# Optimization experiments

Measured on AMD Instinct MI355X. Metric: run time of the kernel, lower is better.

The kernel has to match this reference:

```python
import jax, jax.numpy as jnp
import numpy as np

B, T, C = 4, 2048, 1024
H, D = 16, 64          # n_head, head_size; H*D == C
FF = 4 * C             # compute_layer_scaling * n_embed
EPS = 1e-5


def layernorm(x, g, b):
    mu = jnp.mean(x, axis=-1, keepdims=True)
    var = jnp.var(x, axis=-1, keepdims=True)
    return (x - mu) * jax.lax.rsqrt(var + EPS) * g + b


def setup_inputs() -> dict:
    key = jax.random.key(0)
    ks = jax.random.split(key, 12)
    s_c = 1.0 / np.sqrt(C)
    s_ff = 1.0 / np.sqrt(FF)
    return {
        "x": jax.random.normal(ks[0], (B, T, C), dtype=jnp.float32),
        # per-head Q/K/V weights, stacked: [H, C, D] (Linear with bias=False)
        "Wq": jax.random.normal(ks[1], (H, C, D), dtype=jnp.float32) * s_c,
        "Wk": jax.random.normal(ks[2], (H, C, D), dtype=jnp.float32) * s_c,
        "Wv": jax.random.normal(ks[3], (H, C, D), dtype=jnp.float32) * s_c,
        "Wproj": jax.random.normal(ks[4], (C, C), dtype=jnp.float32) * s_c,
        "bproj": jnp.zeros((C,), dtype=jnp.float32),
        "W1": jax.random.normal(ks[5], (C, FF), dtype=jnp.float32) * s_c,
        "b1": jnp.zeros((FF,), dtype=jnp.float32),
        "W2": jax.random.normal(ks[6], (FF, FF), dtype=jnp.float32) * s_ff,
        "b2": jnp.zeros((FF,), dtype=jnp.float32),
        "W3": jax.random.normal(ks[7], (FF, C), dtype=jnp.float32) * s_ff,
        "b3": jnp.zeros((C,), dtype=jnp.float32),
        "ln1_g": jnp.ones((C,), dtype=jnp.float32),
        "ln1_b": jnp.zeros((C,), dtype=jnp.float32),
        "ln2_g": jnp.ones((C,), dtype=jnp.float32),
        "ln2_b": jnp.zeros((C,), dtype=jnp.float32),
    }


def reference(x, Wq, Wk, Wv, Wproj, bproj, W1, b1, W2, b2, W3, b3,
              ln1_g, ln1_b, ln2_g, ln2_b):
    # --- multi-head causal self-attention (pre-LN) ---
    h = layernorm(x, ln1_g, ln1_b)
    q = jnp.einsum("btc,hcd->bhtd", h, Wq)
    k = jnp.einsum("btc,hcd->bhtd", h, Wk)
    v = jnp.einsum("btc,hcd->bhtd", h, Wv)
    # NOTE: original scales by n_embed**-0.5 (C from x.shape), not head_size
    scores = jnp.einsum("bhtd,bhsd->bhts", q, k) * (C ** -0.5)
    causal = jnp.tril(jnp.ones((T, T), dtype=bool))
    scores = jnp.where(causal, scores, -jnp.inf)
    wei = jax.nn.softmax(scores, axis=-1)          # dropout p=0 -> identity
    attn = jnp.einsum("bhts,bhsd->bhtd", wei, v)
    attn = attn.transpose(0, 2, 1, 3).reshape(B, T, C)  # concat heads
    x = x + attn @ Wproj + bproj
    # --- feed-forward (pre-LN): C -> FF -> relu -> FF -> relu -> C ---
    h2 = layernorm(x, ln2_g, ln2_b)
    h2 = jax.nn.relu(h2 @ W1 + b1)
    h2 = jax.nn.relu(h2 @ W2 + b2)
    x = x + h2 @ W3 + b3
    return x
```

## Files before the change

kernel.cpp:

```cpp
#include <hip/hip_runtime.h>

typedef __bf16 bf16;
typedef bf16  bf16x8 __attribute__((ext_vector_type(8)));
typedef bf16  bf16x4 __attribute__((ext_vector_type(4)));
typedef float f32x4  __attribute__((ext_vector_type(4)));

#define T_SEQ 2048

__device__ __forceinline__ void gload_lds16(const bf16* g, bf16* l) {
    __builtin_amdgcn_global_load_lds(
        (const __attribute__((address_space(1))) unsigned int*)g,
        (__attribute__((address_space(3))) unsigned int*)l,
        16, 0, 0);
}

#define VMCNT(n) asm volatile("s_waitcnt vmcnt(" #n ")" ::: "memory")
#define BAR() do { asm volatile("" ::: "memory"); __builtin_amdgcn_s_barrier(); \
                   asm volatile("" ::: "memory"); } while (0)

__global__ __launch_bounds__(256) void transpose_f32_bf16(
    const float* __restrict__ in, bf16* __restrict__ out, int R, int Cc, int ldo)
{
    __shared__ float tile[32][33];
    const int bx = blockIdx.x * 32;
    const int by = blockIdx.y * 32;
    const long bi = (long)blockIdx.z * R * Cc;
    const long bo = (long)blockIdx.z * Cc * ldo;
    const int tx = threadIdx.x, ty = threadIdx.y;
#pragma unroll
    for (int i = 0; i < 4; ++i)
        tile[ty + i * 8][tx] = in[bi + (long)(by + ty + i * 8) * Cc + bx + tx];
    __syncthreads();
#pragma unroll
    for (int i = 0; i < 4; ++i)
        out[bo + (long)(bx + ty + i * 8) * ldo + by + tx] = (bf16)tile[tx][ty + i * 8];
}

__global__ __launch_bounds__(256) void transpose_bf16(
    const bf16* __restrict__ in, bf16* __restrict__ out, int ldi, int ldo)
{
    __shared__ bf16 tile[32][33];
    const int bx = blockIdx.x * 32;
    const int by = blockIdx.y * 32;
    const int tx = threadIdx.x, ty = threadIdx.y;
#pragma unroll
    for (int i = 0; i < 4; ++i)
        tile[ty + i * 8][tx] = in[(long)(by + ty + i * 8) * ldi + bx + tx];
    __syncthreads();
#pragma unroll
    for (int i = 0; i < 4; ++i)
        out[(long)(bx + ty + i * 8) * ldo + by + tx] = tile[tx][ty + i * 8];
}

__global__ __launch_bounds__(256) void ln_kernel(
    const float* __restrict__ x, const float* __restrict__ g,
    const float* __restrict__ bb, bf16* __restrict__ out)
{
    const long row = blockIdx.x;
    const int tid = threadIdx.x;
    const float4 v = ((const float4*)(x + row * 1024))[tid];
    float s  = v.x + v.y + v.z + v.w;
    float s2 = v.x * v.x + v.y * v.y + v.z * v.z + v.w * v.w;
#pragma unroll
    for (int off = 32; off >= 1; off >>= 1) {
        s  += __shfl_xor(s,  off, 64);
        s2 += __shfl_xor(s2, off, 64);
    }
    __shared__ float red[8];
    const int wid = tid >> 6;
    if ((tid & 63) == 0) { red[wid] = s; red[4 + wid] = s2; }
    __syncthreads();
    s  = red[0] + red[1] + red[2] + red[3];
    s2 = red[4] + red[5] + red[6] + red[7];
    const float mu   = s * (1.f / 1024.f);
    const float rstd = rsqrtf(s2 * (1.f / 1024.f) - mu * mu + 1e-5f);
    const float4 gv = ((const float4*)g)[tid];
    const float4 bv = ((const float4*)bb)[tid];
    bf16x4 ov;
    ov[0] = (bf16)((v.x - mu) * rstd * gv.x + bv.x);
    ov[1] = (bf16)((v.y - mu) * rstd * gv.y + bv.y);
    ov[2] = (bf16)((v.z - mu) * rstd * gv.z + bv.z);
    ov[3] = (bf16)((v.w - mu) * rstd * gv.w + bv.w);
    *(bf16x4*)(out + row * 1024 + tid * 4) = ov;
}

__global__ __launch_bounds__(256) void ln_kernel_b(
    const bf16* __restrict__ x, const float* __restrict__ g,
    const float* __restrict__ bb, bf16* __restrict__ out)
{
    const long row = blockIdx.x;
    const int tid = threadIdx.x;
    const bf16x4 vb = ((const bf16x4*)(x + row * 1024))[tid];
    const float v0 = (float)vb[0], v1 = (float)vb[1];
    const float v2 = (float)vb[2], v3 = (float)vb[3];
    float s  = v0 + v1 + v2 + v3;
    float s2 = v0 * v0 + v1 * v1 + v2 * v2 + v3 * v3;
#pragma unroll
    for (int off = 32; off >= 1; off >>= 1) {
        s  += __shfl_xor(s,  off, 64);
        s2 += __shfl_xor(s2, off, 64);
    }
    __shared__ float red[8];
    const int wid = tid >> 6;
    if ((tid & 63) == 0) { red[wid] = s; red[4 + wid] = s2; }
    __syncthreads();
    s  = red[0] + red[1] + red[2] + red[3];
    s2 = red[4] + red[5] + red[6] + red[7];
    const float mu   = s * (1.f / 1024.f);
    const float rstd = rsqrtf(s2 * (1.f / 1024.f) - mu * mu + 1e-5f);
    const float4 gv = ((const float4*)g)[tid];
    const float4 bv = ((const float4*)bb)[tid];
    bf16x4 ov;
    ov[0] = (bf16)((v0 - mu) * rstd * gv.x + bv.x);
    ov[1] = (bf16)((v1 - mu) * rstd * gv.y + bv.y);
    ov[2] = (bf16)((v2 - mu) * rstd * gv.z + bv.z);
    ov[3] = (bf16)((v3 - mu) * rstd * gv.w + bv.w);
    *(bf16x4*)(out + row * 1024 + tid * 4) = ov;
}

#define LOADA(BUFP, QM) do {                                                   \
    const char* ab_ = (BUFP) + (size_t)((wr * 64 + (QM) * 128 + fr) * 128);    \
    _Pragma("unroll") for (int m_ = 0; m_ < 4; ++m_) {                         \
        af[m_][0] = *(const bf16x8*)(ab_ + m_ * 2048 + so0);                   \
        af[m_][1] = *(const bf16x8*)(ab_ + m_ * 2048 + so1); } } while (0)

#define LOADB(BUFP, QN, DST) do {                                              \
    const char* bb_ = (BUFP) + (size_t)((wc * 32 + (QN) * 128 + fr) * 128);    \
    _Pragma("unroll") for (int n_ = 0; n_ < 2; ++n_) {                         \
        DST[n_][0] = *(const bf16x8*)(bb_ + n_ * 2048 + so0);                  \
        DST[n_][1] = *(const bf16x8*)(bb_ + n_ * 2048 + so1); } } while (0)

#define MMA(ACC, BSET) do { __builtin_amdgcn_s_setprio(1);                     \
    _Pragma("unroll") for (int m_ = 0; m_ < 4; ++m_)                           \
    _Pragma("unroll") for (int n_ = 0; n_ < 2; ++n_) {                         \
        ACC[m_][n_] = __builtin_amdgcn_mfma_f32_16x16x32_bf16(                 \
            af[m_][0], BSET[n_][0], ACC[m_][n_], 0, 0, 0);                     \
        ACC[m_][n_] = __builtin_amdgcn_mfma_f32_16x16x32_bf16(                 \
            af[m_][1], BSET[n_][1], ACC[m_][n_], 0, 0, 0); }                   \
    __builtin_amdgcn_s_setprio(0); } while (0)

#define TB_DEEP(W1N, W3N, ISSN, ISSC) do {                                     \
    const char* abuf = cAs + ((size_t)cur << 15);                              \
    const char* bbuf = cBs + ((size_t)cur << 15);                              \
    const long kb  = (long)(k + 1) * 64;                                       \
    const long kb2 = (long)(k + 2) * 64;                                       \
    LOADA(abuf, 0);                                                            \
    LOADB(bbuf, 0, bfv0);                                                      \
    if (ISSN) stageB(nxt, 0, kb);                                 \
    BAR(); MMA(a00, bfv0); BAR();                                              \
    LOADB(bbuf, 1, bfv1);                                                      \
    if (ISSN) stageA(nxt, 1, kb);                                 \
    VMCNT(W1N);                                                                \
    BAR(); MMA(a01, bfv1); BAR();                                              \
    LOADA(abuf, 1);                                                            \
    if (ISSC) stageA(cur, 0, kb2);                                \
    BAR(); MMA(a11, bfv1); BAR();                                              \
    if (ISSC) stageB(cur, 1, kb2);                                \
    VMCNT(W3N);                                                                \
    BAR(); MMA(a10, bfv0); BAR(); } while (0)

template <int MODE>
__global__ __launch_bounds__(512, 1) void gemm256(
    const bf16* __restrict__ A, const bf16* __restrict__ Bt,
    const float* __restrict__ bias, const float* __restrict__ resid,
    void* __restrict__ outp, int M, int N, int K, int nbn)
{
    extern __shared__ __align__(16) char smem[];
    char* cAs = smem;
    char* cBs = smem + 65536;

    const int tid = threadIdx.x;
    const int wid = tid >> 6, lane = tid & 63;
    const int wr = wid >> 2, wc = wid & 3;
    const int fr = lane & 15, fq = lane >> 4;

    const int nwg = gridDim.x;
    const int cpx = nwg >> 3;
    const int b0  = blockIdx.x;
    const int bid = (b0 & 7) * cpx + (b0 >> 3);
    const long bm = bid / nbn, bn = bid % nbn;
    const long bmrow = bm * 256, bnrow = bn * 256;

    const int srow0 = wid * 8 + (lane >> 3);
    const int sslot = (lane & 7) ^ (lane >> 3);
    auto stageA = [&](int buf, int h, long kt) {
        const bf16* g = A + (size_t)(bmrow + h * 128 + srow0) * K + kt + sslot * 8;
        char* l = cAs + ((size_t)buf << 15) + h * 16384 + (size_t)wid * 1024;
        gload_lds16(g, (bf16*)l);
        gload_lds16(g + (size_t)64 * K, (bf16*)(l + 8192));
    };
    auto stageB = [&](int buf, int h, long kt) {
        const bf16* g = Bt + (size_t)(bnrow + h * 128 + srow0) * K + kt + sslot * 8;
        char* l = cBs + ((size_t)buf << 15) + h * 16384 + (size_t)wid * 1024;
        gload_lds16(g, (bf16*)l);
        gload_lds16(g + (size_t)64 * K, (bf16*)(l + 8192));
    };

    const int sx  = fr & 7;
    const int so0 = ((fq) ^ sx) * 16;
    const int so1 = ((4 + fq) ^ sx) * 16;

    bf16x8 af[4][2], bfv0[2][2], bfv1[2][2];
    f32x4 a00[4][2], a01[4][2], a11[4][2], a10[4][2];
#pragma unroll
    for (int m = 0; m < 4; ++m)
#pragma unroll
        for (int n = 0; n < 2; ++n) {
            a00[m][n] = {0.f, 0.f, 0.f, 0.f}; a01[m][n] = {0.f, 0.f, 0.f, 0.f};
            a11[m][n] = {0.f, 0.f, 0.f, 0.f}; a10[m][n] = {0.f, 0.f, 0.f, 0.f};
        }

    stageA(0, 0, 0);
    stageB(0, 1, 0);
    stageB(0, 0, 0);
    stageA(0, 1, 0);
    stageA(1, 0, 64);
    stageB(1, 1, 64);
    VMCNT(6);
    BAR();

    const int NT = K >> 6;
    int cur, nxt;
    int k = 0;
    for (; k < NT - 2; ++k) {
        cur = k & 1; nxt = cur ^ 1;
        TB_DEEP(8, 6, true, true);
    }
    cur = k & 1; nxt = cur ^ 1;
    TB_DEEP(8, 2, true, false);
    ++k;
    cur = k & 1; nxt = cur ^ 1;
    TB_DEEP(0, 0, false, false);

    auto writeQ = [&](f32x4 (&acc)[4][2], int QM, int QN) {
#pragma unroll
        for (int m = 0; m < 4; ++m) {
            const long row0 = bmrow + wr * 64 + QM * 128 + m * 16 + fq * 4;
#pragma unroll
            for (int n = 0; n < 2; ++n) {
                const long col = bnrow + wc * 32 + QN * 128 + n * 16 + fr;
                const float bv = (MODE == 0) ? 0.f : bias[col];
#pragma unroll
                for (int j = 0; j < 4; ++j) {
                    const long row = row0 + j;
                    float v = acc[m][n][j] + bv;
                    if (MODE == 1) v = fmaxf(v, 0.f);
                    if (MODE == 2) {
                        v += resid[row * N + col];
                        ((float*)outp)[row * N + col] = v;
                    } else {
                        ((bf16*)outp)[row * N + col] = (bf16)v;
                    }
                }
            }
        }
    };
    writeQ(a00, 0, 0); writeQ(a01, 0, 1); writeQ(a11, 1, 1); writeQ(a10, 1, 0);
}

#define TILE_BODY_N(PRE, LAST) do {                                            \
    const char* abuf = cAs + ((size_t)cur << 15);                              \
    const char* bbuf = cBs + ((size_t)cur << 14);                              \
    const long kn = (long)(k + 1) * 64;                                        \
    LOADA(abuf, 0);                                                            \
    LOADB(bbuf, 0, bfv);                                                       \
    if (PRE) { stageA(nxt, 0, kn); stageB(nxt, kn); stageA(nxt, 1, kn);        \
               VMCNT(6); }                                                     \
    else     { VMCNT(0); }                                                     \
    BAR(); MMA(aq0, bfv); BAR();                                               \
    LOADA(abuf, 1);                                                            \
    if (PRE) { VMCNT(2); }                                                     \
    if (!LAST) { BAR(); }                                                      \
    MMA(aq1, bfv);                                                             \
    if (!LAST) { BAR(); } } while (0)

template <int MODE>
__global__ __launch_bounds__(512, 2) void gemm256n(
    const bf16* __restrict__ A, const bf16* __restrict__ Bt,
    const float* __restrict__ bias, const void* __restrict__ resid,
    void* __restrict__ outp, int M, int N, int K, int nbn)
{
    extern __shared__ __align__(16) char smem[];
    char* cAs = smem;
    char* cBs = smem + 65536;

    const int tid = threadIdx.x;
    const int wid = tid >> 6, lane = tid & 63;
    const int wr = wid >> 2, wc = wid & 3;
    const int fr = lane & 15, fq = lane >> 4;

    const int nwg = gridDim.x;
    const int cpx = nwg >> 3;
    const int b0  = blockIdx.x;
    const int bid = (b0 & 7) * cpx + (b0 >> 3);
    const long bm = bid / nbn, bn = bid % nbn;
    const long bmrow = bm * 256, bnrow = bn * 128;

    const int srow0 = wid * 8 + (lane >> 3);
    const int sslot = (lane & 7) ^ (lane >> 3);
    auto stageA = [&](int buf, int h, long kt) {
        const bf16* g = A + (size_t)(bmrow + h * 128 + srow0) * K + kt + sslot * 8;
        char* l = cAs + ((size_t)buf << 15) + h * 16384 + (size_t)wid * 1024;
        gload_lds16(g, (bf16*)l);
        gload_lds16(g + (size_t)64 * K, (bf16*)(l + 8192));
    };
    auto stageB = [&](int buf, long kt) {
        const bf16* g = Bt + (size_t)(bnrow + srow0) * K + kt + sslot * 8;
        char* l = cBs + ((size_t)buf << 14) + (size_t)wid * 1024;
        gload_lds16(g, (bf16*)l);
        gload_lds16(g + (size_t)64 * K, (bf16*)(l + 8192));
    };

    const int sx  = fr & 7;
    const int so0 = ((fq) ^ sx) * 16;
    const int so1 = ((4 + fq) ^ sx) * 16;

    bf16x8 af[4][2], bfv[2][2];
    f32x4 aq0[4][2], aq1[4][2];
#pragma unroll
    for (int m = 0; m < 4; ++m)
#pragma unroll
        for (int n = 0; n < 2; ++n) {
            aq0[m][n] = {0.f, 0.f, 0.f, 0.f};
            aq1[m][n] = {0.f, 0.f, 0.f, 0.f};
        }

    stageA(0, 0, 0); stageB(0, 0); stageA(0, 1, 0);
    VMCNT(2);
    BAR();

    const int NT = K >> 6;
    int cur = 0, nxt = 1;
    int k = 0;
    for (; k < NT - 1; ++k) {
        cur = k & 1; nxt = cur ^ 1;
        TILE_BODY_N(true, false);
    }
    cur = k & 1; nxt = cur ^ 1;
    TILE_BODY_N(false, true);

    auto writeQ = [&](f32x4 (&acc)[4][2], int QM) {
#pragma unroll
        for (int m = 0; m < 4; ++m) {
            const long row0 = bmrow + wr * 64 + QM * 128 + m * 16 + fq * 4;
#pragma unroll
            for (int n = 0; n < 2; ++n) {
                const long col = bnrow + wc * 32 + n * 16 + fr;
                const float bv = (MODE == 0) ? 0.f : bias[col];
#pragma unroll
                for (int j = 0; j < 4; ++j) {
                    const long row = row0 + j;
                    float v = acc[m][n][j] + bv;
                    if (MODE == 3) {
                        v += ((const float*)resid)[row * N + col];
                        ((bf16*)outp)[row * N + col] = (bf16)v;
                    } else if (MODE == 4) {
                        v += (float)((const bf16*)resid)[row * N + col];
                        ((float*)outp)[row * N + col] = v;
                    } else {
                        ((bf16*)outp)[row * N + col] = (bf16)v;
                    }
                }
            }
        }
    };
    writeQ(aq0, 0); writeQ(aq1, 1);
}

__device__ __forceinline__ void sm_part(
    f32x4* s, float* mj, f32x4* o, f32x4& o_l, bf16* Pp,
    int fr, int fq, int qloc, bool diag)
{
    float v[4][4], mxj[4];
#pragma unroll
    for (int j = 0; j < 4; ++j) {
        const int qg = qloc + fq * 4 + j;
        v[0][j] = s[0][j] * 0.03125f;
        v[1][j] = s[1][j] * 0.03125f;
        v[2][j] = s[2][j] * 0.03125f;
        v[3][j] = s[3][j] * 0.03125f;
        if (diag) {
            if (fr      > qg) v[0][j] = -1e30f;
            if (16 + fr > qg) v[1][j] = -1e30f;
            if (32 + fr > qg) v[2][j] = -1e30f;
            if (48 + fr > qg) v[3][j] = -1e30f;
        }
        float mx = fmaxf(fmaxf(v[0][j], v[1][j]), fmaxf(v[2][j], v[3][j]));
#pragma unroll
        for (int off = 1; off <= 8; off <<= 1) mx = fmaxf(mx, __shfl_xor(mx, off, 16));
        mxj[j] = mx;
    }
    float need = fmaxf(fmaxf(mxj[0] - mj[0], mxj[1] - mj[1]),
                       fmaxf(mxj[2] - mj[2], mxj[3] - mj[3]));
    if (__any(need > 8.f)) {
#pragma unroll
        for (int j = 0; j < 4; ++j) {
            const float mn   = fmaxf(mj[j], mxj[j]);
            const float corr = __expf(mj[j] - mn);
            mj[j] = mn;
#pragma unroll
            for (int nd = 0; nd < 4; ++nd) o[nd][j] *= corr;
            o_l[j] *= corr;
        }
    }
#pragma unroll
    for (int j = 0; j < 4; ++j) {
        bf16* prow = Pp + (fq * 4 + j) * 72;
        prow[fr]      = (bf16)__expf(v[0][j] - mj[j]);
        prow[16 + fr] = (bf16)__expf(v[1][j] - mj[j]);
        prow[32 + fr] = (bf16)__expf(v[2][j] - mj[j]);
        prow[48 + fr] = (bf16)__expf(v[3][j] - mj[j]);
    }
}

__device__ __forceinline__ void attn_step(
    const bf16* __restrict__ Ks, const bf16* __restrict__ Vt,
    bf16* __restrict__ Pp, const bf16x8* qf,
    f32x4* o, f32x4& o_l, float* mj, const bf16x8 onesf,
    int fr, int fq, int qloc, bool diag)
{
    f32x4 s[4];
#pragma unroll
    for (int n = 0; n < 4; ++n) s[n] = {0.f, 0.f, 0.f, 0.f};
    __builtin_amdgcn_s_setprio(1);
#pragma unroll
    for (int n = 0; n < 4; ++n) {
        const int t  = n * 16 + fr;
        const int sw = ((t ^ (t >> 3)) & 7) << 4;
        const bf16x8 kf0 = *(const bf16x8*)((const char*)Ks + t * 128 + ((fq * 16) ^ sw));
        const bf16x8 kf1 = *(const bf16x8*)((const char*)Ks + t * 128 + ((64 + fq * 16) ^ sw));
        s[n] = __builtin_amdgcn_mfma_f32_16x16x32_bf16(qf[0], kf0, s[n], 0, 0, 0);
        s[n] = __builtin_amdgcn_mfma_f32_16x16x32_bf16(qf[1], kf1, s[n], 0, 0, 0);
    }
    __builtin_amdgcn_s_setprio(0);
    sm_part(s, mj, o, o_l, Pp, fr, fq, qloc, diag);
    asm volatile("s_waitcnt lgkmcnt(0)" ::: "memory");
    __builtin_amdgcn_sched_barrier(0);
    const bf16x8 pf0 = *(const bf16x8*)(Pp + fr * 72 + fq * 8);
    const bf16x8 pf1 = *(const bf16x8*)(Pp + fr * 72 + 32 + fq * 8);
    __builtin_amdgcn_s_setprio(1);
#pragma unroll
    for (int nd = 0; nd < 4; ++nd) {
        const int dd = nd * 16 + fr;
        const int sw = ((dd ^ (dd >> 3)) & 7) << 4;
        const bf16x8 vf0 = *(const bf16x8*)((const char*)Vt + dd * 128 + ((fq * 16) ^ sw));
        const bf16x8 vf1 = *(const bf16x8*)((const char*)Vt + dd * 128 + ((64 + fq * 16) ^ sw));
        o[nd] = __builtin_amdgcn_mfma_f32_16x16x32_bf16(pf0, vf0, o[nd], 0, 0, 0);
        o[nd] = __builtin_amdgcn_mfma_f32_16x16x32_bf16(pf1, vf1, o[nd], 0, 0, 0);
    }
    o_l = __builtin_amdgcn_mfma_f32_16x16x32_bf16(pf0, onesf, o_l, 0, 0, 0);
    o_l = __builtin_amdgcn_mfma_f32_16x16x32_bf16(pf1, onesf, o_l, 0, 0, 0);
    __builtin_amdgcn_s_setprio(0);
}

__device__ __forceinline__ void attn_step2(
    const bf16* __restrict__ Ks, const bf16* __restrict__ Vt,
    bf16* __restrict__ PpA, bf16* __restrict__ PpB,
    const bf16x8* qfA, const bf16x8* qfB,
    f32x4* oA, f32x4& olA, float* mA,
    f32x4* oB, f32x4& olB, float* mB,
    const bf16x8 onesf, int fr, int fq, int qloc, bool diagA)
{
    f32x4 sA[4], sB[4];
#pragma unroll
    for (int n = 0; n < 4; ++n) { sA[n] = {0.f, 0.f, 0.f, 0.f}; sB[n] = {0.f, 0.f, 0.f, 0.f}; }
    __builtin_amdgcn_s_setprio(1);
#pragma unroll
    for (int n = 0; n < 4; ++n) {
        const int t  = n * 16 + fr;
        const int sw = ((t ^ (t >> 3)) & 7) << 4;
        const bf16x8 kf0 = *(const bf16x8*)((const char*)Ks + t * 128 + ((fq * 16) ^ sw));
        const bf16x8 kf1 = *(const bf16x8*)((const char*)Ks + t * 128 + ((64 + fq * 16) ^ sw));
        sA[n] = __builtin_amdgcn_mfma_f32_16x16x32_bf16(qfA[0], kf0, sA[n], 0, 0, 0);
        sA[n] = __builtin_amdgcn_mfma_f32_16x16x32_bf16(qfA[1], kf1, sA[n], 0, 0, 0);
        sB[n] = __builtin_amdgcn_mfma_f32_16x16x32_bf16(qfB[0], kf0, sB[n], 0, 0, 0);
        sB[n] = __builtin_amdgcn_mfma_f32_16x16x32_bf16(qfB[1], kf1, sB[n], 0, 0, 0);
    }
    __builtin_amdgcn_s_setprio(0);
    sm_part(sA, mA, oA, olA, PpA, fr, fq, qloc, diagA);
    sm_part(sB, mB, oB, olB, PpB, fr, fq, qloc, false);
    asm volatile("s_waitcnt lgkmcnt(0)" ::: "memory");
    __builtin_amdgcn_sched_barrier(0);
    const bf16x8 pfA0 = *(const bf16x8*)(PpA + fr * 72 + fq * 8);
    const bf16x8 pfA1 = *(const bf16x8*)(PpA + fr * 72 + 32 + fq * 8);
    const bf16x8 pfB0 = *(const bf16x8*)(PpB + fr * 72 + fq * 8);
    const bf16x8 pfB1 = *(const bf16x8*)(PpB + fr * 72 + 32 + fq * 8);
    __builtin_amdgcn_s_setprio(1);
#pragma unroll
    for (int nd = 0; nd < 4; ++nd) {
        const int dd = nd * 16 + fr;
        const int sw = ((dd ^ (dd >> 3)) & 7) << 4;
        const bf16x8 vf0 = *(const bf16x8*)((const char*)Vt + dd * 128 + ((fq * 16) ^ sw));
        const bf16x8 vf1 = *(const bf16x8*)((const char*)Vt + dd * 128 + ((64 + fq * 16) ^ sw));
        oA[nd] = __builtin_amdgcn_mfma_f32_16x16x32_bf16(pfA0, vf0, oA[nd], 0, 0, 0);
        oA[nd] = __builtin_amdgcn_mfma_f32_16x16x32_bf16(pfA1, vf1, oA[nd], 0, 0, 0);
        oB[nd] = __builtin_amdgcn_mfma_f32_16x16x32_bf16(pfB0, vf0, oB[nd], 0, 0, 0);
        oB[nd] = __builtin_amdgcn_mfma_f32_16x16x32_bf16(pfB1, vf1, oB[nd], 0, 0, 0);
    }
    olA = __builtin_amdgcn_mfma_f32_16x16x32_bf16(pfA0, onesf, olA, 0, 0, 0);
    olA = __builtin_amdgcn_mfma_f32_16x16x32_bf16(pfA1, onesf, olA, 0, 0, 0);
    olB = __builtin_amdgcn_mfma_f32_16x16x32_bf16(pfB0, onesf, olB, 0, 0, 0);
    olB = __builtin_amdgcn_mfma_f32_16x16x32_bf16(pfB1, onesf, olB, 0, 0, 0);
    __builtin_amdgcn_s_setprio(0);
}

__global__ __launch_bounds__(256) void attn_kernel(
    const bf16* __restrict__ qkv, const bf16* __restrict__ vt,
    bf16* __restrict__ out)
{
    const int pair = blockIdx.x;
    const int h = blockIdx.y, b = blockIdx.z;
    const int tid = threadIdx.x, wid = tid >> 6, lane = tid & 63;
    const int fr = lane & 15, fq = lane >> 4;
    const int jA = pair, jB = 31 - pair;
    const bf16* baseQ = qkv + ((long)b * T_SEQ) * 3072 + h * 64;
    const bf16* baseK = baseQ + 1024;
    const bf16* baseV = vt + (long)(h * 64) * 8192 + (long)b * T_SEQ;

    __shared__ __align__(16) bf16 Ks[2][64 * 64];
    __shared__ __align__(16) bf16 Vs[2][64 * 64];
    __shared__ __align__(16) bf16 Plds[2][4][16 * 72];

    const int qrA = jA * 64 + wid * 16 + fr;
    const int qrB = jB * 64 + wid * 16 + fr;
    bf16x8 qfA[2], qfB[2];
#pragma unroll
    for (int kk = 0; kk < 2; ++kk) {
        qfA[kk] = *(const bf16x8*)(baseQ + (long)qrA * 3072 + kk * 32 + fq * 8);
        qfB[kk] = *(const bf16x8*)(baseQ + (long)qrB * 3072 + kk * 32 + fq * 8);
    }

    bf16x8 onesf;
    {
        const bf16 ov = (fr == 0) ? (bf16)1.f : (bf16)0.f;
#pragma unroll
        for (int e = 0; e < 8; ++e) onesf[e] = ov;
    }

    f32x4 oA[4], oB[4], olA, olB;
    float mA[4], mB[4];
#pragma unroll
    for (int nd = 0; nd < 4; ++nd) { oA[nd] = {0.f, 0.f, 0.f, 0.f}; oB[nd] = {0.f, 0.f, 0.f, 0.f}; }
    olA = {0.f, 0.f, 0.f, 0.f}; olB = {0.f, 0.f, 0.f, 0.f};
#pragma unroll
    for (int j = 0; j < 4; ++j) { mA[j] = -1e30f; mB[j] = -1e30f; }

    const int t_p0 = wid * 16 + (lane >> 3);
    const int t_p1 = t_p0 + 8;
    const int kcb0 = ((lane & 7) * 16) ^ (((t_p0 ^ (t_p0 >> 3)) & 7) << 4);
    const int kcb1 = ((lane & 7) * 16) ^ (((t_p1 ^ (t_p1 >> 3)) & 7) << 4);

    bf16* PA = &Plds[0][wid][0];
    bf16* PB = &Plds[1][wid][0];

    auto stage = [&](int buf, int c) {
        const long s0 = (long)c * 64;
        gload_lds16(baseK + (s0 + t_p0) * 3072 + (kcb0 >> 1), &Ks[buf][(wid * 2) * 512]);
        gload_lds16(baseK + (s0 + t_p1) * 3072 + (kcb1 >> 1), &Ks[buf][(wid * 2 + 1) * 512]);
        gload_lds16(baseV + (long)t_p0 * 8192 + s0 + (kcb0 >> 1), &Vs[buf][(wid * 2) * 512]);
        gload_lds16(baseV + (long)t_p1 * 8192 + s0 + (kcb1 >> 1), &Vs[buf][(wid * 2 + 1) * 512]);
    };

    const int nch = jB + 1;
    stage(0, 0);
    for (int c = 0; c < nch; ++c) {
        const int cur = c & 1;
        if (c + 1 < nch) { stage(cur ^ 1, c + 1); VMCNT(4); }
        else             { VMCNT(0); }
        BAR();
        if (c <= jA)
            attn_step2(Ks[cur], Vs[cur], PA, PB, qfA, qfB,
                       oA, olA, mA, oB, olB, mB, onesf, fr, fq, wid * 16, c == jA);
        else
            attn_step(Ks[cur], Vs[cur], PB, qfB, oB, olB, mB, onesf,
                      fr, fq, wid * 16, c == jB);
        BAR();
    }

#pragma unroll
    for (int j = 0; j < 4; ++j) {
        const float lA = __shfl(olA[j], lane & 48, 64);
        const float lB = __shfl(olB[j], lane & 48, 64);
        const float rA = 1.f / lA, rB = 1.f / lB;
        const long rowA = (long)b * T_SEQ + jA * 64 + wid * 16 + fq * 4 + j;
        const long rowB = (long)b * T_SEQ + jB * 64 + wid * 16 + fq * 4 + j;
#pragma unroll
        for (int nd = 0; nd < 4; ++nd) {
            out[rowA * 1024 + h * 64 + nd * 16 + fr] = (bf16)(oA[nd][j] * rA);
            out[rowB * 1024 + h * 64 + nd * 16 + fr] = (bf16)(oB[nd][j] * rB);
        }
    }
}

extern "C" void kernel_launch(void* const* d_in, const int* in_sizes, int n_in,
                              void* d_out, int out_size, void* d_ws, size_t ws_size,
                              hipStream_t stream)
{
    const float* x     = (const float*)d_in[0];
    const float* Wq    = (const float*)d_in[1];
    const float* Wk    = (const float*)d_in[2];
    const float* Wv    = (const float*)d_in[3];
    const float* Wproj = (const float*)d_in[4];
    const float* bproj = (const float*)d_in[5];
    const float* W1    = (const float*)d_in[6];
    const float* b1    = (const float*)d_in[7];
    const float* W2    = (const float*)d_in[8];
    const float* b2    = (const float*)d_in[9];
    const float* W3    = (const float*)d_in[10];
    const float* b3    = (const float*)d_in[11];
    const float* ln1g  = (const float*)d_in[12];
    const float* ln1b  = (const float*)d_in[13];
    const float* ln2g  = (const float*)d_in[14];
    const float* ln2b  = (const float*)d_in[15];

    char* ws = (char*)d_ws;
    size_t off = 0;
    auto alloc = [&](size_t bytes) {
        void* p = ws + off;
        off += (bytes + 255) & ~(size_t)255;
        return p;
    };
    bf16* Wqkv_t  = (bf16*)alloc(3072ul * 1024 * 2);
    bf16* Wproj_t = (bf16*)alloc(1024ul * 1024 * 2);
    bf16* W1_t    = (bf16*)alloc(4096ul * 1024 * 2);
    bf16* W2_t    = (bf16*)alloc(4096ul * 4096 * 2);
    bf16* W3_t    = (bf16*)alloc(1024ul * 4096 * 2);
    bf16* hbuf    = (bf16*)alloc(8192ul * 1024 * 2);
    bf16* x1b     = (bf16*)alloc(8192ul * 1024 * 2);
    bf16* a1      = (bf16*)alloc(8192ul * 4096 * 2);
    char* R1      = (char*)alloc(8192ul * 4096 * 2);
    bf16* qkvb    = (bf16*)R1;
    bf16* attnb   = (bf16*)(R1 + 8192ul * 3072 * 2);
    bf16* a2      = (bf16*)R1;
    bf16* vt      = a1;

    hipFuncSetAttribute(reinterpret_cast<const void*>(&gemm256<1>),
                        hipFuncAttributeMaxDynamicSharedMemorySize, 131072);
    hipFuncSetAttribute(reinterpret_cast<const void*>(&gemm256n<0>),
                        hipFuncAttributeMaxDynamicSharedMemorySize, 98304);
    hipFuncSetAttribute(reinterpret_cast<const void*>(&gemm256n<3>),
                        hipFuncAttributeMaxDynamicSharedMemorySize, 98304);
    hipFuncSetAttribute(reinterpret_cast<const void*>(&gemm256n<4>),
                        hipFuncAttributeMaxDynamicSharedMemorySize, 98304);

    const dim3 tb(32, 8);
    transpose_f32_bf16<<<dim3(2, 32, 16), tb, 0, stream>>>(Wq, Wqkv_t,                1024, 64, 1024);
    transpose_f32_bf16<<<dim3(2, 32, 16), tb, 0, stream>>>(Wk, Wqkv_t + 1024l * 1024, 1024, 64, 1024);
    transpose_f32_bf16<<<dim3(2, 32, 16), tb, 0, stream>>>(Wv, Wqkv_t + 2048l * 1024, 1024, 64, 1024);
    transpose_f32_bf16<<<dim3(32, 32, 1),   tb, 0, stream>>>(Wproj, Wproj_t, 1024, 1024, 1024);
    transpose_f32_bf16<<<dim3(128, 32, 1),  tb, 0, stream>>>(W1, W1_t, 1024, 4096, 1024);
    transpose_f32_bf16<<<dim3(128, 128, 1), tb, 0, stream>>>(W2, W2_t, 4096, 4096, 4096);
    transpose_f32_bf16<<<dim3(32, 128, 1),  tb, 0, stream>>>(W3, W3_t, 4096, 1024, 4096);

    ln_kernel<<<8192, 256, 0, stream>>>(x, ln1g, ln1b, hbuf);
    gemm256n<0><<<768, 512, 98304, stream>>>(hbuf, Wqkv_t, nullptr, nullptr, qkvb,
                                             8192, 3072, 1024, 24);
    transpose_bf16<<<dim3(32, 256), tb, 0, stream>>>(qkvb + 2048, vt, 3072, 8192);
    attn_kernel<<<dim3(16, 16, 4), 256, 0, stream>>>(qkvb, vt, attnb);
    gemm256n<3><<<256, 512, 98304, stream>>>(attnb, Wproj_t, bproj, x, x1b,
                                             8192, 1024, 1024, 8);
    ln_kernel_b<<<8192, 256, 0, stream>>>(x1b, ln2g, ln2b, hbuf);
    gemm256<1><<<512, 512, 131072, stream>>>(hbuf, W1_t, b1, nullptr, a1,
                                             8192, 4096, 1024, 16);
    gemm256<1><<<512, 512, 131072, stream>>>(a1, W2_t, b2, nullptr, a2,
                                             8192, 4096, 4096, 16);
    gemm256n<4><<<256, 512, 98304, stream>>>(a2, W3_t, b3, x1b, (float*)d_out,
                                             8192, 1024, 4096, 8);
}
```

Baseline: 665.5 us.

## Process two causal query-tile pairs per attention block to reuse K/V tiles

Each attention block now handles four query tiles (two balanced causal pairs) sharing the same staged K/V chunks, halving the grid and the K/V load traffic. P scratch moves to dynamic shared memory sized for four tiles. This raises register and LDS use per block, which may reduce occupancy and parallelism with only 512 blocks.

Result: slower. 730.2 us (+9.7%).

```diff
diff --git a/kernel.cpp b/kernel.cpp
--- a/kernel.cpp
+++ b/kernel.cpp
@@ -508,26 +508,28 @@
     const bf16* __restrict__ qkv, const bf16* __restrict__ vt,
     bf16* __restrict__ out)
 {
-    const int pair = blockIdx.x;
+    const int p = blockIdx.x;
     const int h = blockIdx.y, b = blockIdx.z;
     const int tid = threadIdx.x, wid = tid >> 6, lane = tid & 63;
     const int fr = lane & 15, fq = lane >> 4;
-    const int jA = pair, jB = 31 - pair;
+    const int jA1 = p, jB1 = 31 - p;
+    const int jA2 = p + 8, jB2 = 23 - p;
     const bf16* baseQ = qkv + ((long)b * T_SEQ) * 3072 + h * 64;
     const bf16* baseK = baseQ + 1024;
     const bf16* baseV = vt + (long)(h * 64) * 8192 + (long)b * T_SEQ;
 
-    __shared__ __align__(16) bf16 Ks[2][64 * 64];
-    __shared__ __align__(16) bf16 Vs[2][64 * 64];
-    __shared__ __align__(16) bf16 Plds[2][4][16 * 72];
-
-    const int qrA = jA * 64 + wid * 16 + fr;
-    const int qrB = jB * 64 + wid * 16 + fr;
-    bf16x8 qfA[2], qfB[2];
+    extern __shared__ __align__(16) char asmem[];
+    bf16* Ks = (bf16*)asmem;
+    bf16* Vs = (bf16*)(asmem + 16384);
+    bf16* Pl = (bf16*)(asmem + 32768);
+
+    bf16x8 qfA1[2], qfB1[2], qfA2[2], qfB2[2];
 #pragma unroll
     for (int kk = 0; kk < 2; ++kk) {
-        qfA[kk] = *(const bf16x8*)(baseQ + (long)qrA * 3072 + kk * 32 + fq * 8);
-        qfB[kk] = *(const bf16x8*)(baseQ + (long)qrB * 3072 + kk * 32 + fq * 8);
+        qfA1[kk] = *(const bf16x8*)(baseQ + (long)(jA1 * 64 + wid * 16 + fr) * 3072 + kk * 32 + fq * 8);
+        qfB1[kk] = *(const bf16x8*)(baseQ + (long)(jB1 * 64 + wid * 16 + fr) * 3072 + kk * 32 + fq * 8);
+        qfA2[kk] = *(const bf16x8*)(baseQ + (long)(jA2 * 64 + wid * 16 + fr) * 3072 + kk * 32 + fq * 8);
+        qfB2[kk] = *(const bf16x8*)(baseQ + (long)(jB2 * 64 + wid * 16 + fr) * 3072 + kk * 32 + fq * 8);
     }
 
     bf16x8 onesf;
@@ -537,59 +539,74 @@
         for (int e = 0; e < 8; ++e) onesf[e] = ov;
     }
 
-    f32x4 oA[4], oB[4], olA, olB;
-    float mA[4], mB[4];
-#pragma unroll
-    for (int nd = 0; nd < 4; ++nd) { oA[nd] = {0.f, 0.f, 0.f, 0.f}; oB[nd] = {0.f, 0.f, 0.f, 0.f}; }
-    olA = {0.f, 0.f, 0.f, 0.f}; olB = {0.f, 0.f, 0.f, 0.f};
-#pragma unroll
-    for (int j = 0; j < 4; ++j) { mA[j] = -1e30f; mB[j] = -1e30f; }
+    f32x4 oA1[4], oB1[4], oA2[4], oB2[4], olA1, olB1, olA2, olB2;
+    float mA1[4], mB1[4], mA2[4], mB2[4];
+#pragma unroll
+    for (int nd = 0; nd < 4; ++nd) {
+        oA1[nd] = {0.f, 0.f, 0.f, 0.f}; oB1[nd] = {0.f, 0.f, 0.f, 0.f};
+        oA2[nd] = {0.f, 0.f, 0.f, 0.f}; oB2[nd] = {0.f, 0.f, 0.f, 0.f};
+    }
+    olA1 = {0.f, 0.f, 0.f, 0.f}; olB1 = {0.f, 0.f, 0.f, 0.f};
+    olA2 = {0.f, 0.f, 0.f, 0.f}; olB2 = {0.f, 0.f, 0.f, 0.f};
+#pragma unroll
+    for (int j = 0; j < 4; ++j) { mA1[j] = -1e30f; mB1[j] = -1e30f;
+                                  mA2[j] = -1e30f; mB2[j] = -1e30f; }
 
     const int t_p0 = wid * 16 + (lane >> 3);
     const int t_p1 = t_p0 + 8;
     const int kcb0 = ((lane & 7) * 16) ^ (((t_p0 ^ (t_p0 >> 3)) & 7) << 4);
     const int kcb1 = ((lane & 7) * 16) ^ (((t_p1 ^ (t_p1 >> 3)) & 7) << 4);
 
-    bf16* PA = &Plds[0][wid][0];
-    bf16* PB = &Plds[1][wid][0];
+    bf16* PA1 = Pl + (0 * 4 + wid) * 1152;
+    bf16* PB1 = Pl + (1 * 4 + wid) * 1152;
+    bf16* PA2 = Pl + (2 * 4 + wid) * 1152;
+    bf16* PB2 = Pl + (3 * 4 + wid) * 1152;
 
     auto stage = [&](int buf, int c) {
         const long s0 = (long)c * 64;
-        gload_lds16(baseK + (s0 + t_p0) * 3072 + (kcb0 >> 1), &Ks[buf][(wid * 2) * 512]);
-        gload_lds16(baseK + (s0 + t_p1) * 3072 + (kcb1 >> 1), &Ks[buf][(wid * 2 + 1) * 512]);
-        gload_lds16(baseV + (long)t_p0 * 8192 + s0 + (kcb0 >> 1), &Vs[buf][(wid * 2) * 512]);
-        gload_lds16(baseV + (long)t_p1 * 8192 + s0 + (kcb1 >> 1), &Vs[buf][(wid * 2 + 1) * 512]);
-    };
-
-    const int nch = jB + 1;
+        gload_lds16(baseK + (s0 + t_p0) * 3072 + (kcb0 >> 1), Ks + buf * 4096 + (wid * 2) * 512);
+        gload_lds16(baseK + (s0 + t_p1) * 3072 + (kcb1 >> 1), Ks + buf * 4096 + (wid * 2 + 1) * 512);
+        gload_lds16(baseV + (long)t_p0 * 8192 + s0 + (kcb0 >> 1), Vs + buf * 4096 + (wid * 2) * 512);
+        gload_lds16(baseV + (long)t_p1 * 8192 + s0 + (kcb1 >> 1), Vs + buf * 4096 + (wid * 2 + 1) * 512);
+    };
+
+    const int nch = jB1 + 1;
     stage(0, 0);
     for (int c = 0; c < nch; ++c) {
         const int cur = c & 1;
         if (c + 1 < nch) { stage(cur ^ 1, c + 1); VMCNT(4); }
         else             { VMCNT(0); }
         BAR();
-        if (c <= jA)
-            attn_step2(Ks[cur], Vs[cur], PA, PB, qfA, qfB,
-                       oA, olA, mA, oB, olB, mB, onesf, fr, fq, wid * 16, c == jA);
+        const bf16* Kc = Ks + cur * 4096;
+        const bf16* Vc = Vs + cur * 4096;
+        if (c <= jA1)
+            attn_step2(Kc, Vc, PA1, PB1, qfA1, qfB1,
+                       oA1, olA1, mA1, oB1, olB1, mB1, onesf, fr, fq, wid * 16, c == jA1);
         else
-            attn_step(Ks[cur], Vs[cur], PB, qfB, oB, olB, mB, onesf,
-                      fr, fq, wid * 16, c == jB);
+            attn_step(Kc, Vc, PB1, qfB1, oB1, olB1, mB1, onesf,
+                      fr, fq, wid * 16, c == jB1);
+        if (c <= jA2)
+            attn_step2(Kc, Vc, PA2, PB2, qfA2, qfB2,
+                       oA2, olA2, mA2, oB2, olB2, mB2, onesf, fr, fq, wid * 16, c == jA2);
+        else if (c <= jB2)
+            attn_step(Kc, Vc, PB2, qfB2, oB2, olB2, mB2, onesf,
+                      fr, fq, wid * 16, c == jB2);
         BAR();
     }
 
-#pragma unroll
-    for (int j = 0; j < 4; ++j) {
-        const float lA = __shfl(olA[j], lane & 48, 64);
-        const float lB = __shfl(olB[j], lane & 48, 64);
-        const float rA = 1.f / lA, rB = 1.f / lB;
-        const long rowA = (long)b * T_SEQ + jA * 64 + wid * 16 + fq * 4 + j;
-        const long rowB = (long)b * T_SEQ + jB * 64 + wid * 16 + fq * 4 + j;
-#pragma unroll
-        for (int nd = 0; nd < 4; ++nd) {
-            out[rowA * 1024 + h * 64 + nd * 16 + fr] = (bf16)(oA[nd][j] * rA);
-            out[rowB * 1024 + h * 64 + nd * 16 + fr] = (bf16)(oB[nd][j] * rB);
+    auto writeO = [&](f32x4* o, f32x4& ol, int jq) {
+#pragma unroll
+        for (int j = 0; j < 4; ++j) {
+            const float l = __shfl(ol[j], lane & 48, 64);
+            const float r = 1.f / l;
+            const long row = (long)b * T_SEQ + jq * 64 + wid * 16 + fq * 4 + j;
+#pragma unroll
+            for (int nd = 0; nd < 4; ++nd)
+                out[row * 1024 + h * 64 + nd * 16 + fr] = (bf16)(o[nd][j] * r);
         }
-    }
+    };
+    writeO(oA1, olA1, jA1); writeO(oB1, olB1, jB1);
+    writeO(oA2, olA2, jA2); writeO(oB2, olB2, jB2);
 }
 
 extern "C" void kernel_launch(void* const* d_in, const int* in_sizes, int n_in,
@@ -642,6 +659,8 @@
                         hipFuncAttributeMaxDynamicSharedMemorySize, 98304);
     hipFuncSetAttribute(reinterpret_cast<const void*>(&gemm256n<4>),
                         hipFuncAttributeMaxDynamicSharedMemorySize, 98304);
+    hipFuncSetAttribute(reinterpret_cast<const void*>(&attn_kernel),
+                        hipFuncAttributeMaxDynamicSharedMemorySize, 69632);
 
     const dim3 tb(32, 8);
     transpose_f32_bf16<<<dim3(2, 32, 16), tb, 0, stream>>>(Wq, Wqkv_t,                1024, 64, 1024);
@@ -656,7 +675,7 @@
     gemm256n<0><<<768, 512, 98304, stream>>>(hbuf, Wqkv_t, nullptr, nullptr, qkvb,
                                              8192, 3072, 1024, 24);
     transpose_bf16<<<dim3(32, 256), tb, 0, stream>>>(qkvb + 2048, vt, 3072, 8192);
-    attn_kernel<<<dim3(16, 16, 4), 256, 0, stream>>>(qkvb, vt, attnb);
+    attn_kernel<<<dim3(8, 16, 4), 256, 69632, stream>>>(qkvb, vt, attnb);
     gemm256n<3><<<256, 512, 98304, stream>>>(attnb, Wproj_t, bproj, x, x1b,
                                              8192, 1024, 1024, 8);
     ln_kernel_b<<<8192, 256, 0, stream>>>(x1b, ln2g, ln2b, hbuf);
```

## Fuse V transpose into QKV GEMM epilogue and shrink attention P buffer

Applied to the files above, without the earlier changes.

The QKV GEMM gains a new epilogue mode that writes the V columns directly in transposed layout, which removes the separate bf16 transpose kernel and its extra memory round trip. In attention, the per-wave P scratch is halved to a single buffer that the A and B query halves reuse one after the other, and it now uses an XOR-swizzled 128-byte row layout instead of padded rows. Launch bounds request 4 blocks per CU, aiming for higher occupancy. The transposed V stores from the GEMM are strided, so they are uncoalesced, and reusing one P buffer serialises the two softmax passes.

Result: slower. 893.6 us (+34.3%).

```diff
diff --git a/kernel.cpp b/kernel.cpp
--- a/kernel.cpp
+++ b/kernel.cpp
@@ -34,22 +34,6 @@
 #pragma unroll
     for (int i = 0; i < 4; ++i)
         out[bo + (long)(bx + ty + i * 8) * ldo + by + tx] = (bf16)tile[tx][ty + i * 8];
-}
-
-__global__ __launch_bounds__(256) void transpose_bf16(
-    const bf16* __restrict__ in, bf16* __restrict__ out, int ldi, int ldo)
-{
-    __shared__ bf16 tile[32][33];
-    const int bx = blockIdx.x * 32;
-    const int by = blockIdx.y * 32;
-    const int tx = threadIdx.x, ty = threadIdx.y;
-#pragma unroll
-    for (int i = 0; i < 4; ++i)
-        tile[ty + i * 8][tx] = in[(long)(by + ty + i * 8) * ldi + bx + tx];
-    __syncthreads();
-#pragma unroll
-    for (int i = 0; i < 4; ++i)
-        out[(long)(bx + ty + i * 8) * ldo + by + tx] = tile[tx][ty + i * 8];
 }
 
 __global__ __launch_bounds__(256) void ln_kernel(
@@ -346,7 +330,7 @@
 #pragma unroll
             for (int n = 0; n < 2; ++n) {
                 const long col = bnrow + wc * 32 + n * 16 + fr;
-                const float bv = (MODE == 0) ? 0.f : bias[col];
+                const float bv = (MODE == 0 || MODE == 5) ? 0.f : bias[col];
 #pragma unroll
                 for (int j = 0; j < 4; ++j) {
                     const long row = row0 + j;
@@ -357,6 +341,11 @@
                     } else if (MODE == 4) {
                         v += (float)((const bf16*)resid)[row * N + col];
                         ((float*)outp)[row * N + col] = v;
+                    } else if (MODE == 5) {
+                        if (col < 2048)
+                            ((bf16*)outp)[row * N + col] = (bf16)v;
+                        else
+                            ((bf16*)resid)[(col - 2048) * 8192 + row] = (bf16)v;
                     } else {
                         ((bf16*)outp)[row * N + col] = (bf16)v;
                     }
@@ -405,13 +394,20 @@
     }
 #pragma unroll
     for (int j = 0; j < 4; ++j) {
-        bf16* prow = Pp + (fq * 4 + j) * 72;
-        prow[fr]      = (bf16)__expf(v[0][j] - mj[j]);
-        prow[16 + fr] = (bf16)__expf(v[1][j] - mj[j]);
-        prow[32 + fr] = (bf16)__expf(v[2][j] - mj[j]);
-        prow[48 + fr] = (bf16)__expf(v[3][j] - mj[j]);
-    }
-}
+        const int r = fq * 4 + j;
+        char* prow = (char*)Pp + r * 128;
+        const int sw = (r & 7) << 4;
+        *(bf16*)(prow + ((fr * 2) ^ sw))      = (bf16)__expf(v[0][j] - mj[j]);
+        *(bf16*)(prow + ((32 + fr * 2) ^ sw)) = (bf16)__expf(v[1][j] - mj[j]);
+        *(bf16*)(prow + ((64 + fr * 2) ^ sw)) = (bf16)__expf(v[2][j] - mj[j]);
+        *(bf16*)(prow + ((96 + fr * 2) ^ sw)) = (bf16)__expf(v[3][j] - mj[j]);
+    }
+}
+
+#define PLOAD(P0, P1, PP) do {                                                 \
+    const int swr_ = (fr & 7) << 4;                                            \
+    P0 = *(const bf16x8*)((const char*)(PP) + fr * 128 + ((fq * 16) ^ swr_));  \
+    P1 = *(const bf16x8*)((const char*)(PP) + fr * 128 + ((64 + fq * 16) ^ swr_)); } while (0)
 
 __device__ __forceinline__ void attn_step(
     const bf16* __restrict__ Ks, const bf16* __restrict__ Vt,
@@ -436,8 +432,8 @@
     sm_part(s, mj, o, o_l, Pp, fr, fq, qloc, diag);
     asm volatile("s_waitcnt lgkmcnt(0)" ::: "memory");
     __builtin_amdgcn_sched_barrier(0);
-    const bf16x8 pf0 = *(const bf16x8*)(Pp + fr * 72 + fq * 8);
-    const bf16x8 pf1 = *(const bf16x8*)(Pp + fr * 72 + 32 + fq * 8);
+    bf16x8 pf0, pf1;
+    PLOAD(pf0, pf1, Pp);
     __builtin_amdgcn_s_setprio(1);
 #pragma unroll
     for (int nd = 0; nd < 4; ++nd) {
@@ -455,7 +451,7 @@
 
 __device__ __forceinline__ void attn_step2(
     const bf16* __restrict__ Ks, const bf16* __restrict__ Vt,
-    bf16* __restrict__ PpA, bf16* __restrict__ PpB,
+    bf16* __restrict__ Pp,
     const bf16x8* qfA, const bf16x8* qfB,
     f32x4* oA, f32x4& olA, float* mA,
     f32x4* oB, f32x4& olB, float* mB,
@@ -477,14 +473,16 @@
         sB[n] = __builtin_amdgcn_mfma_f32_16x16x32_bf16(qfB[1], kf1, sB[n], 0, 0, 0);
     }
     __builtin_amdgcn_s_setprio(0);
-    sm_part(sA, mA, oA, olA, PpA, fr, fq, qloc, diagA);
-    sm_part(sB, mB, oB, olB, PpB, fr, fq, qloc, false);
+    sm_part(sA, mA, oA, olA, Pp, fr, fq, qloc, diagA);
     asm volatile("s_waitcnt lgkmcnt(0)" ::: "memory");
     __builtin_amdgcn_sched_barrier(0);
-    const bf16x8 pfA0 = *(const bf16x8*)(PpA + fr * 72 + fq * 8);
-    const bf16x8 pfA1 = *(const bf16x8*)(PpA + fr * 72 + 32 + fq * 8);
-    const bf16x8 pfB0 = *(const bf16x8*)(PpB + fr * 72 + fq * 8);
-    const bf16x8 pfB1 = *(const bf16x8*)(PpB + fr * 72 + 32 + fq * 8);
+    bf16x8 pfA0, pfA1;
+    PLOAD(pfA0, pfA1, Pp);
+    sm_part(sB, mB, oB, olB, Pp, fr, fq, qloc, false);
+    asm volatile("s_waitcnt lgkmcnt(0)" ::: "memory");
+    __builtin_amdgcn_sched_barrier(0);
+    bf16x8 pfB0, pfB1;
+    PLOAD(pfB0, pfB1, Pp);
     __builtin_amdgcn_s_setprio(1);
 #pragma unroll
     for (int nd = 0; nd < 4; ++nd) {
@@ -504,7 +502,7 @@
     __builtin_amdgcn_s_setprio(0);
 }
 
-__global__ __launch_bounds__(256) void attn_kernel(
+__global__ __launch_bounds__(256, 4) void attn_kernel(
     const bf16* __restrict__ qkv, const bf16* __restrict__ vt,
     bf16* __restrict__ out)
 {
@@ -519,7 +517,7 @@
 
     __shared__ __align__(16) bf16 Ks[2][64 * 64];
     __shared__ __align__(16) bf16 Vs[2][64 * 64];
-    __shared__ __align__(16) bf16 Plds[2][4][16 * 72];
+    __shared__ __align__(16) bf16 Pl[4][1024];
 
     const int qrA = jA * 64 + wid * 16 + fr;
     const int qrB = jB * 64 + wid * 16 + fr;
@@ -550,8 +548,7 @@
     const int kcb0 = ((lane & 7) * 16) ^ (((t_p0 ^ (t_p0 >> 3)) & 7) << 4);
     const int kcb1 = ((lane & 7) * 16) ^ (((t_p1 ^ (t_p1 >> 3)) & 7) << 4);
 
-    bf16* PA = &Plds[0][wid][0];
-    bf16* PB = &Plds[1][wid][0];
+    bf16* P = &Pl[wid][0];
 
     auto stage = [&](int buf, int c) {
         const long s0 = (long)c * 64;
@@ -569,10 +566,10 @@
         else             { VMCNT(0); }
         BAR();
         if (c <= jA)
-            attn_step2(Ks[cur], Vs[cur], PA, PB, qfA, qfB,
+            attn_step2(Ks[cur], Vs[cur], P, qfA, qfB,
                        oA, olA, mA, oB, olB, mB, onesf, fr, fq, wid * 16, c == jA);
         else
-            attn_step(Ks[cur], Vs[cur], PB, qfB, oB, olB, mB, onesf,
+            attn_step(Ks[cur], Vs[cur], P, qfB, oB, olB, mB, onesf,
                       fr, fq, wid * 16, c == jB);
         BAR();
     }
@@ -636,7 +633,7 @@
 
     hipFuncSetAttribute(reinterpret_cast<const void*>(&gemm256<1>),
                         hipFuncAttributeMaxDynamicSharedMemorySize, 131072);
-    hipFuncSetAttribute(reinterpret_cast<const void*>(&gemm256n<0>),
+    hipFuncSetAttribute(reinterpret_cast<const void*>(&gemm256n<5>),
                         hipFuncAttributeMaxDynamicSharedMemorySize, 98304);
     hipFuncSetAttribute(reinterpret_cast<const void*>(&gemm256n<3>),
                         hipFuncAttributeMaxDynamicSharedMemorySize, 98304);
@@ -653,9 +650,8 @@
     transpose_f32_bf16<<<dim3(32, 128, 1),  tb, 0, stream>>>(W3, W3_t, 4096, 1024, 4096);
 
     ln_kernel<<<8192, 256, 0, stream>>>(x, ln1g, ln1b, hbuf);
-    gemm256n<0><<<768, 512, 98304, stream>>>(hbuf, Wqkv_t, nullptr, nullptr, qkvb,
+    gemm256n<5><<<768, 512, 98304, stream>>>(hbuf, Wqkv_t, nullptr, vt, qkvb,
                                              8192, 3072, 1024, 24);
-    transpose_bf16<<<dim3(32, 256), tb, 0, stream>>>(qkvb + 2048, vt, 3072, 8192);
     attn_kernel<<<dim3(16, 16, 4), 256, 0, stream>>>(qkvb, vt, attnb);
     gemm256n<3><<<256, 512, 98304, stream>>>(attnb, Wproj_t, bproj, x, x1b,
                                              8192, 1024, 1024, 8);
```

## Restructure 256x256 GEMM warp tiling to contiguous 128x64 per-wave tiles

Applied to the files above, without the earlier changes.

Changes the gemm256 kernel's per-wave work from four separate quadrant sub-tiles to one contiguous 128x64 tile per wave, with 4x4 MFMA blocks per half and a K-split into two 32-wide steps. The pipeline goes from a deeper three-stage prefetch to a simpler double-buffered schedule that issues the next tile's B then A loads between MMA phases. This aims to cut LDS fragment loads per MFMA and simplify the barrier schedule. The cost is less prefetch depth, which may expose global-load latency.

Result: no change. 676.9 us (+1.7%).

```diff
diff --git a/kernel.cpp b/kernel.cpp
--- a/kernel.cpp
+++ b/kernel.cpp
@@ -118,46 +118,38 @@
     *(bf16x4*)(out + row * 1024 + tid * 4) = ov;
 }
 
-#define LOADA(BUFP, QM) do {                                                   \
-    const char* ab_ = (BUFP) + (size_t)((wr * 64 + (QM) * 128 + fr) * 128);    \
-    _Pragma("unroll") for (int m_ = 0; m_ < 4; ++m_) {                         \
-        af[m_][0] = *(const bf16x8*)(ab_ + m_ * 2048 + so0);                   \
-        af[m_][1] = *(const bf16x8*)(ab_ + m_ * 2048 + so1); } } while (0)
-
-#define LOADB(BUFP, QN, DST) do {                                              \
-    const char* bb_ = (BUFP) + (size_t)((wc * 32 + (QN) * 128 + fr) * 128);    \
-    _Pragma("unroll") for (int n_ = 0; n_ < 2; ++n_) {                         \
-        DST[n_][0] = *(const bf16x8*)(bb_ + n_ * 2048 + so0);                  \
-        DST[n_][1] = *(const bf16x8*)(bb_ + n_ * 2048 + so1); } } while (0)
-
-#define MMA(ACC, BSET) do { __builtin_amdgcn_s_setprio(1);                     \
+#define LA2(MH, SOX) do {                                                      \
     _Pragma("unroll") for (int m_ = 0; m_ < 4; ++m_)                           \
-    _Pragma("unroll") for (int n_ = 0; n_ < 2; ++n_) {                         \
-        ACC[m_][n_] = __builtin_amdgcn_mfma_f32_16x16x32_bf16(                 \
-            af[m_][0], BSET[n_][0], ACC[m_][n_], 0, 0, 0);                     \
-        ACC[m_][n_] = __builtin_amdgcn_mfma_f32_16x16x32_bf16(                 \
-            af[m_][1], BSET[n_][1], ACC[m_][n_], 0, 0, 0); }                   \
+        af[m_] = *(const bf16x8*)(abuf + ((MH) * 64 + m_ * 16 + fr) * 128 + (SOX)); } while (0)
+
+#define LB2(SOX) do {                                                          \
+    _Pragma("unroll") for (int n_ = 0; n_ < 4; ++n_)                           \
+        bfv[n_] = *(const bf16x8*)(bbuf + (n_ * 16 + fr) * 128 + (SOX)); } while (0)
+
+#define MMA16(MH) do { __builtin_amdgcn_s_setprio(1);                          \
+    _Pragma("unroll") for (int m_ = 0; m_ < 4; ++m_)                           \
+    _Pragma("unroll") for (int n_ = 0; n_ < 4; ++n_)                           \
+        acc[(MH) * 4 + m_][n_] = __builtin_amdgcn_mfma_f32_16x16x32_bf16(      \
+            af[m_], bfv[n_], acc[(MH) * 4 + m_][n_], 0, 0, 0);                 \
     __builtin_amdgcn_s_setprio(0); } while (0)
 
-#define TB_DEEP(W1N, W3N, ISSN, ISSC) do {                                     \
-    const char* abuf = cAs + ((size_t)cur << 15);                              \
-    const char* bbuf = cBs + ((size_t)cur << 15);                              \
-    const long kb  = (long)(k + 1) * 64;                                       \
-    const long kb2 = (long)(k + 2) * 64;                                       \
-    LOADA(abuf, 0);                                                            \
-    LOADB(bbuf, 0, bfv0);                                                      \
-    if (ISSN) stageB(nxt, 0, kb);                                 \
-    BAR(); MMA(a00, bfv0); BAR();                                              \
-    LOADB(bbuf, 1, bfv1);                                                      \
-    if (ISSN) stageA(nxt, 1, kb);                                 \
-    VMCNT(W1N);                                                                \
-    BAR(); MMA(a01, bfv1); BAR();                                              \
-    LOADA(abuf, 1);                                                            \
-    if (ISSC) stageA(cur, 0, kb2);                                \
-    BAR(); MMA(a11, bfv1); BAR();                                              \
-    if (ISSC) stageB(cur, 1, kb2);                                \
+#define TB2(W0N, W3N, ISS) do {                                                \
+    const char* abuf = cAs + ((size_t)cur << 15) + (size_t)wr * 16384;         \
+    const char* bbuf = cBs + ((size_t)cur << 15) + (size_t)(wc >> 1) * 16384   \
+                       + (size_t)((wc & 1) * 64) * 128;                        \
+    const long kb = (long)(k + 1) * 64;                                        \
+    LA2(0, so0); LB2(so0);                                                     \
+    if (ISS) { stageB(nxt, 0, kb); stageB(nxt, 1, kb); }                       \
+    VMCNT(W0N);                                                                \
+    BAR(); MMA16(0); BAR();                                                    \
+    LA2(1, so0);                                                               \
+    if (ISS) { stageA(nxt, 0, kb); stageA(nxt, 1, kb); }                       \
+    BAR(); MMA16(1); BAR();                                                    \
+    LA2(0, so1); LB2(so1);                                                     \
+    BAR(); MMA16(0); BAR();                                                    \
+    LA2(1, so1);                                                               \
     VMCNT(W3N);                                                                \
-    BAR(); MMA(a10, bfv0); BAR(); } while (0)
+    BAR(); MMA16(1); BAR(); } while (0)
 
 template <int MODE>
 __global__ __launch_bounds__(512, 1) void gemm256(
@@ -200,45 +192,35 @@
     const int so0 = ((fq) ^ sx) * 16;
     const int so1 = ((4 + fq) ^ sx) * 16;
 
-    bf16x8 af[4][2], bfv0[2][2], bfv1[2][2];
-    f32x4 a00[4][2], a01[4][2], a11[4][2], a10[4][2];
-#pragma unroll
-    for (int m = 0; m < 4; ++m)
-#pragma unroll
-        for (int n = 0; n < 2; ++n) {
-            a00[m][n] = {0.f, 0.f, 0.f, 0.f}; a01[m][n] = {0.f, 0.f, 0.f, 0.f};
-            a11[m][n] = {0.f, 0.f, 0.f, 0.f}; a10[m][n] = {0.f, 0.f, 0.f, 0.f};
-        }
-
-    stageA(0, 0, 0);
-    stageB(0, 1, 0);
-    stageB(0, 0, 0);
-    stageA(0, 1, 0);
-    stageA(1, 0, 64);
-    stageB(1, 1, 64);
-    VMCNT(6);
+    bf16x8 af[4], bfv[4];
+    f32x4 acc[8][4];
+#pragma unroll
+    for (int m = 0; m < 8; ++m)
+#pragma unroll
+        for (int n = 0; n < 4; ++n) acc[m][n] = {0.f, 0.f, 0.f, 0.f};
+
+    stageB(0, 0, 0); stageB(0, 1, 0);
+    stageA(0, 0, 0); stageA(0, 1, 0);
+    VMCNT(2);
     BAR();
 
     const int NT = K >> 6;
     int cur, nxt;
     int k = 0;
-    for (; k < NT - 2; ++k) {
+    for (; k < NT - 1; ++k) {
         cur = k & 1; nxt = cur ^ 1;
-        TB_DEEP(8, 6, true, true);
+        TB2(4, 2, true);
     }
     cur = k & 1; nxt = cur ^ 1;
-    TB_DEEP(8, 2, true, false);
-    ++k;
-    cur = k & 1; nxt = cur ^ 1;
-    TB_DEEP(0, 0, false, false);
-
-    auto writeQ = [&](f32x4 (&acc)[4][2], int QM, int QN) {
-#pragma unroll
-        for (int m = 0; m < 4; ++m) {
-            const long row0 = bmrow + wr * 64 + QM * 128 + m * 16 + fq * 4;
-#pragma unroll
-            for (int n = 0; n < 2; ++n) {
-                const long col = bnrow + wc * 32 + QN * 128 + n * 16 + fr;
+    TB2(0, 0, false);
+
+    auto writeQ = [&]() {
+#pragma unroll
+        for (int m = 0; m < 8; ++m) {
+            const long row0 = bmrow + wr * 128 + m * 16 + fq * 4;
+#pragma unroll
+            for (int n = 0; n < 4; ++n) {
+                const long col = bnrow + wc * 64 + n * 16 + fr;
                 const float bv = (MODE == 0) ? 0.f : bias[col];
 #pragma unroll
                 for (int j = 0; j < 4; ++j) {
@@ -255,8 +237,29 @@
             }
         }
     };
-    writeQ(a00, 0, 0); writeQ(a01, 0, 1); writeQ(a11, 1, 1); writeQ(a10, 1, 0);
-}
+    writeQ();
+}
+
+#define LOADA(BUFP, QM) do {                                                   \
+    const char* ab_ = (BUFP) + (size_t)((wr * 64 + (QM) * 128 + fr) * 128);    \
+    _Pragma("unroll") for (int m_ = 0; m_ < 4; ++m_) {                         \
+        af[m_][0] = *(const bf16x8*)(ab_ + m_ * 2048 + so0);                   \
+        af[m_][1] = *(const bf16x8*)(ab_ + m_ * 2048 + so1); } } while (0)
+
+#define LOADB(BUFP, QN, DST) do {                                              \
+    const char* bb_ = (BUFP) + (size_t)((wc * 32 + (QN) * 128 + fr) * 128);    \
+    _Pragma("unroll") for (int n_ = 0; n_ < 2; ++n_) {                         \
+        DST[n_][0] = *(const bf16x8*)(bb_ + n_ * 2048 + so0);                  \
+        DST[n_][1] = *(const bf16x8*)(bb_ + n_ * 2048 + so1); } } while (0)
+
+#define MMA(ACC, BSET) do { __builtin_amdgcn_s_setprio(1);                     \
+    _Pragma("unroll") for (int m_ = 0; m_ < 4; ++m_)                           \
+    _Pragma("unroll") for (int n_ = 0; n_ < 2; ++n_) {                         \
+        ACC[m_][n_] = __builtin_amdgcn_mfma_f32_16x16x32_bf16(                 \
+            af[m_][0], BSET[n_][0], ACC[m_][n_], 0, 0, 0);                     \
+        ACC[m_][n_] = __builtin_amdgcn_mfma_f32_16x16x32_bf16(                 \
+            af[m_][1], BSET[n_][1], ACC[m_][n_], 0, 0, 0); }                   \
+    __builtin_amdgcn_s_setprio(0); } while (0)
 
 #define TILE_BODY_N(PRE, LAST) do {                                            \
     const char* abuf = cAs + ((size_t)cur << 15);                              \
```
